# Performance work log

Hardware: AMD Instinct MI355X
Metric: run time of the kernel (lower is better)

Reference implementation:

```python
import jax, jax.numpy as jnp
import numpy as np

B, L, D = 32768, 256, 16  # batch, chain length, bond dim; physical dim d=2


def setup_inputs() -> dict:
    key = jax.random.key(0)
    k_phi, k_first, k_mid, k_last = jax.random.split(key, 4)
    scale = 1.0 / np.sqrt(2.0 * D)  # variance-preserving chain
    phi_batch = jax.random.normal(k_phi, (B, L, 2), dtype=jnp.float32)
    core_first = jax.random.normal(k_first, (2, D), dtype=jnp.float32) * scale
    cores_mid = jax.random.normal(k_mid, (L - 2, D, 2, D), dtype=jnp.float32) * scale
    core_last = jax.random.normal(k_last, (D, 2), dtype=jnp.float32) * scale
    out_bias = jnp.zeros((), dtype=jnp.float32)
    return {
        "phi_batch": phi_batch,
        "core_first": core_first,
        "cores_mid": cores_mid,
        "core_last": core_last,
        "out_bias": out_bias,
    }


def reference(phi_batch, core_first, cores_mid, core_last, out_bias):
    # MPS / tensor-train contraction, batched over samples.
    # Each sample contracts feature vectors phi[i] (len-2) into the physical
    # index of core i, then chains the resulting D x D matrices via a
    # left-to-right bond-space matvec (what cotengra would find per-sample).
    # v0: [B, D] = phi[:,0] contracted with first core [2, D]
    v0 = jnp.einsum("bp,pd->bd", phi_batch[:, 0], core_first)

    # middle features, scan-major layout: [L-2, B, 2]
    phis_mid = jnp.swapaxes(phi_batch[:, 1:-1], 0, 1)

    def step(v, xs):
        phi_t, core = xs  # phi_t: [B, 2], core: [D, 2, D]
        # contract bond then physical index; never materialize [B, D, D]
        u = jnp.einsum("bq,qpr->bpr", v, core)   # [B, 2, D]
        v_new = jnp.einsum("bp,bpr->br", phi_t, u)  # [B, D]
        return v_new, None

    v, _ = jax.lax.scan(step, v0, (phis_mid, cores_mid))

    # close the chain with last core [D, 2] and last feature [B, 2]
    out = jnp.einsum("bq,qp,bp->b", v, core_last, phi_batch[:, -1])
    return out + out_bias
```

## Files before the change

### kernel.cpp

```cpp
#include <hip/hip_runtime.h>
#include <stdint.h>


typedef short  bf16x8 __attribute__((ext_vector_type(8)));
typedef float  f32x4  __attribute__((ext_vector_type(4)));
typedef int    i32x4  __attribute__((ext_vector_type(4)));
typedef unsigned int u32;

#define NFWD 128
#define NBWD 126
#define BWD_OFF (NFWD*2*64)

#if __has_builtin(__builtin_amdgcn_perm)
#define PACK_HI(hi, lo) ((int)__builtin_amdgcn_perm((u32)(hi), (u32)(lo), 0x07060302u))
#else
#define PACK_HI(hi, lo) ((int)(((u32)(hi) & 0xFFFF0000u) | ((u32)(lo) >> 16)))
#endif

__device__ __forceinline__ u32 rne_bump(u32 u){
  return u + 0x7FFFu + ((u >> 16) & 1u);
}

__global__ void build_frags(const float* __restrict__ cm, i32x4* __restrict__ ws)
{
  const int bid  = blockIdx.x;
  const int p    = threadIdx.x >> 6;
  const int lane = threadIdx.x & 63;
  const int m    = lane & 15;
  const int g    = lane >> 4;
  const bool fwd = bid < NFWD;
  const int slot = fwd ? bid : (bid - NFWD);
  const int t    = fwd ? bid : (253 - slot);
  i32x4* dst = ws + (fwd ? 0 : BWD_OFF) + (slot*2 + p)*64 + lane;
  i32x4 w;
  #pragma unroll
  for(int d=0; d<4; ++d){
    u32 h[2];
    #pragma unroll
    for(int e=0; e<2; ++e){
      const int j = 2*d + e;
      const int k = g*8 + j;
      const int q = k & 15;
      const int lohalf = k >> 4;
      const int ci = fwd ? ((((t*16 + q)*2) + p)*16 + m)
                         : ((((t*16 + m)*2) + p)*16 + q);
      const float c = cm[ci];
      const u32 u  = __float_as_uint(c);
      const u32 a  = rne_bump(u);
      const float hif = __uint_as_float(a & 0xFFFF0000u);
      const u32 b  = rne_bump(__float_as_uint(c - hif));
      h[e] = lohalf ? (b >> 16) : (a >> 16);
    }
    w[d] = (int)(h[0] | (h[1] << 16));
  }
  *dst = w;
}

__global__ __launch_bounds__(256) void mps_chain(
  const float* __restrict__ phi,
  const float* __restrict__ core_first,
  const float* __restrict__ core_last,
  const float* __restrict__ bias,
  const i32x4* __restrict__ ws,
  float* __restrict__ out)
{
  const int lane = threadIdx.x & 63;
  const int wv   = threadIdx.x >> 6;
  const int b0   = blockIdx.x * 32;
  const int n    = lane & 15;
  const int g    = lane >> 4;
  const int s_in = (wv & 1)*16 + n;
  const bool isFwd = (wv < 2);
  const bool hiSel = (g < 2);
  const int addrA  = (n + 32*(g & 1)) << 2;
  const int addrB  = addrA + 64;

  const float* phiRow = phi + (size_t)(b0 + s_in) * 512;

  __shared__ float red[2][32][20];

  float v[4];
  i32x4 bfrag, bswap;

  auto make_bfrag = [&](){
    const u32 u0 = __float_as_uint(v[0]), u1 = __float_as_uint(v[1]);
    const u32 u2 = __float_as_uint(v[2]), u3 = __float_as_uint(v[3]);
    const float l0 = v[0] - __uint_as_float(u0 & 0xFFFF0000u);
    const float l1 = v[1] - __uint_as_float(u1 & 0xFFFF0000u);
    const float l2 = v[2] - __uint_as_float(u2 & 0xFFFF0000u);
    const float l3 = v[3] - __uint_as_float(u3 & 0xFFFF0000u);
    const int hp01 = PACK_HI(u1, u0);
    const int hp23 = PACK_HI(u3, u2);
    const int lp01 = PACK_HI(__float_as_uint(l1), __float_as_uint(l0));
    const int lp23 = PACK_HI(__float_as_uint(l3), __float_as_uint(l2));
    const int ah0 = __builtin_amdgcn_ds_bpermute(addrA, hp01);
    const int ah1 = __builtin_amdgcn_ds_bpermute(addrA, hp23);
    const int al0 = __builtin_amdgcn_ds_bpermute(addrA, lp01);
    const int al1 = __builtin_amdgcn_ds_bpermute(addrA, lp23);
    const int bh0 = __builtin_amdgcn_ds_bpermute(addrB, hp01);
    const int bh1 = __builtin_amdgcn_ds_bpermute(addrB, hp23);
    const int bl0 = __builtin_amdgcn_ds_bpermute(addrB, lp01);
    const int bl1 = __builtin_amdgcn_ds_bpermute(addrB, lp23);
    bfrag[0] = hiSel ? ah0 : al0;   bswap[0] = hiSel ? al0 : ah0;
    bfrag[1] = hiSel ? ah1 : al1;   bswap[1] = hiSel ? al1 : ah1;
    bfrag[2] = hiSel ? bh0 : bl0;   bswap[2] = hiSel ? bl0 : bh0;
    bfrag[3] = hiSel ? bh1 : bl1;   bswap[3] = hiSel ? bl1 : bh1;
  };

  auto step = [&](const i32x4& a0, const i32x4& a1, float phx, float phy){
    f32x4 acc0 = {0.f,0.f,0.f,0.f};
    f32x4 acc1 = {0.f,0.f,0.f,0.f};
    const bf16x8 bh = __builtin_bit_cast(bf16x8, bfrag);
    const bf16x8 bs = __builtin_bit_cast(bf16x8, bswap);
    acc0 = __builtin_amdgcn_mfma_f32_16x16x32_bf16(__builtin_bit_cast(bf16x8, a0), bh, acc0, 0,0,0);
    acc0 = __builtin_amdgcn_mfma_f32_16x16x32_bf16(__builtin_bit_cast(bf16x8, a0), bs, acc0, 0,0,0);
    acc1 = __builtin_amdgcn_mfma_f32_16x16x32_bf16(__builtin_bit_cast(bf16x8, a1), bh, acc1, 0,0,0);
    acc1 = __builtin_amdgcn_mfma_f32_16x16x32_bf16(__builtin_bit_cast(bf16x8, a1), bs, acc1, 0,0,0);
    v[0] = phx*acc0[0] + phy*acc1[0];
    v[1] = phx*acc0[1] + phy*acc1[1];
    v[2] = phx*acc0[2] + phy*acc1[2];
    v[3] = phx*acc0[3] + phy*acc1[3];
    make_bfrag();
  };

  if (isFwd){
    const i32x4* tab = ws;
    float4 f4a = *(const float4*)phiRow;
    #pragma unroll
    for(int reg=0; reg<4; ++reg){
      const int r = g*4 + reg;
      v[reg] = f4a.x * core_first[r] + f4a.y * core_first[16 + r];
    }
    make_bfrag();
    i32x4 P0 = tab[lane],       P1 = tab[64 + lane];
    i32x4 Q0 = tab[128 + lane], Q1 = tab[192 + lane];
    #pragma unroll 1
    for(int t = 0; t < NFWD; t += 2){
      const float4 f4n = *(const float4*)(phiRow + 2*(t+2));
      step(P0, P1, f4a.z, f4a.w);
      {
        const int sp = (t+2 < NFWD) ? (t+2) : (NFWD-1);
        P0 = tab[sp*128 + lane]; P1 = tab[sp*128 + 64 + lane];
      }
      step(Q0, Q1, f4n.x, f4n.y);
      {
        const int sq = (t+3 < NFWD) ? (t+3) : (NFWD-1);
        Q0 = tab[sq*128 + lane]; Q1 = tab[sq*128 + 64 + lane];
      }
      f4a = f4n;
    }
  } else {
    const i32x4* tab = ws + BWD_OFF;
    float4 f4a = *(const float4*)(phiRow + 508);
    #pragma unroll
    for(int reg=0; reg<4; ++reg){
      const int r = g*4 + reg;
      v[reg] = f4a.z * core_last[2*r] + f4a.w * core_last[2*r + 1];
    }
    make_bfrag();
    i32x4 P0 = tab[lane],       P1 = tab[64 + lane];
    i32x4 Q0 = tab[128 + lane], Q1 = tab[192 + lane];
    float cx = f4a.x, cy = f4a.y;
    #pragma unroll 1
    for(int s = 0; s < NBWD; s += 2){
      const float4 f4n = *(const float4*)(phiRow + 2*(252-s));
      step(P0, P1, cx, cy);
      {
        const int sp = (s+2 < NBWD) ? (s+2) : (NBWD-1);
        P0 = tab[sp*128 + lane]; P1 = tab[sp*128 + 64 + lane];
      }
      step(Q0, Q1, f4n.z, f4n.w);
      {
        const int sq = (s+3 < NBWD) ? (s+3) : (NBWD-1);
        Q0 = tab[sq*128 + lane]; Q1 = tab[sq*128 + 64 + lane];
      }
      cx = f4n.x; cy = f4n.y;
    }
  }

  *(float4*)&red[isFwd ? 0 : 1][s_in][4*g] = make_float4(v[0], v[1], v[2], v[3]);
  __syncthreads();
  if (threadIdx.x < 32){
    const int s = threadIdx.x;
    float acc = bias[0];
    #pragma unroll
    for(int q = 0; q < 16; ++q)
      acc += red[0][s][q] * red[1][s][q];
    out[b0 + s] = acc;
  }
}

extern "C" void kernel_launch(void* const* d_in, const int* in_sizes, int n_in,
                              void* d_out, int out_size, void* d_ws, size_t ws_size,
                              hipStream_t stream)
{
  const float* phi  = (const float*)d_in[0];
  const float* cf   = (const float*)d_in[1];
  const float* cm   = (const float*)d_in[2];
  const float* cl   = (const float*)d_in[3];
  const float* bias = (const float*)d_in[4];
  i32x4* ws = (i32x4*)d_ws;

  build_frags<<<254, 128, 0, stream>>>(cm, ws);
  mps_chain<<<1024, 256, 0, stream>>>(phi, cf, cl, bias, ws, (float*)d_out);
}
```

Measured before the change: 157.1 us.

## Reorder core fragment layout to drop cross-lane bpermutes in chain step

Changes the k-ordering of the prebuilt bf16 hi/lo core fragments so each lane's own packed vector values can feed the MFMA B operand directly. This removes the eight ds_bpermute shuffles and selects on the serial per-step critical path, which now only packs and swaps registers. The prefetch of core fragments and phi values is also deepened from two steps to four, with an explicit tail for the backward chain. The cost is more live registers and a new correctness dependency on the fragment layout matching the MFMA operand mapping.

```diff
diff --git a/kernel.cpp b/kernel.cpp
--- a/kernel.cpp
+++ b/kernel.cpp
@@ -11,11 +11,7 @@
 #define NBWD 126
 #define BWD_OFF (NFWD*2*64)
 
-#if __has_builtin(__builtin_amdgcn_perm)
 #define PACK_HI(hi, lo) ((int)__builtin_amdgcn_perm((u32)(hi), (u32)(lo), 0x07060302u))
-#else
-#define PACK_HI(hi, lo) ((int)(((u32)(hi) & 0xFFFF0000u) | ((u32)(lo) >> 16)))
-#endif
 
 __device__ __forceinline__ u32 rne_bump(u32 u){
   return u + 0x7FFFu + ((u >> 16) & 1u);
@@ -39,9 +35,8 @@
     #pragma unroll
     for(int e=0; e<2; ++e){
       const int j = 2*d + e;
-      const int k = g*8 + j;
-      const int q = k & 15;
-      const int lohalf = k >> 4;
+      const int q = 4*g + (j & 3);
+      const bool hi_part = (j < 4);
       const int ci = fwd ? ((((t*16 + q)*2) + p)*16 + m)
                          : ((((t*16 + m)*2) + p)*16 + q);
       const float c = cm[ci];
@@ -49,7 +44,7 @@
       const u32 a  = rne_bump(u);
       const float hif = __uint_as_float(a & 0xFFFF0000u);
       const u32 b  = rne_bump(__float_as_uint(c - hif));
-      h[e] = lohalf ? (b >> 16) : (a >> 16);
+      h[e] = hi_part ? (a >> 16) : (b >> 16);
     }
     w[d] = (int)(h[0] | (h[1] << 16));
   }
@@ -71,16 +66,13 @@
   const int g    = lane >> 4;
   const int s_in = (wv & 1)*16 + n;
   const bool isFwd = (wv < 2);
-  const bool hiSel = (g < 2);
-  const int addrA  = (n + 32*(g & 1)) << 2;
-  const int addrB  = addrA + 64;
 
   const float* phiRow = phi + (size_t)(b0 + s_in) * 512;
 
   __shared__ float red[2][32][20];
 
   float v[4];
-  i32x4 bfrag, bswap;
+  i32x4 bfr;
 
   auto make_bfrag = [&](){
     const u32 u0 = __float_as_uint(v[0]), u1 = __float_as_uint(v[1]);
@@ -89,29 +81,18 @@
     const float l1 = v[1] - __uint_as_float(u1 & 0xFFFF0000u);
     const float l2 = v[2] - __uint_as_float(u2 & 0xFFFF0000u);
     const float l3 = v[3] - __uint_as_float(u3 & 0xFFFF0000u);
-    const int hp01 = PACK_HI(u1, u0);
-    const int hp23 = PACK_HI(u3, u2);
-    const int lp01 = PACK_HI(__float_as_uint(l1), __float_as_uint(l0));
-    const int lp23 = PACK_HI(__float_as_uint(l3), __float_as_uint(l2));
-    const int ah0 = __builtin_amdgcn_ds_bpermute(addrA, hp01);
-    const int ah1 = __builtin_amdgcn_ds_bpermute(addrA, hp23);
-    const int al0 = __builtin_amdgcn_ds_bpermute(addrA, lp01);
-    const int al1 = __builtin_amdgcn_ds_bpermute(addrA, lp23);
-    const int bh0 = __builtin_amdgcn_ds_bpermute(addrB, hp01);
-    const int bh1 = __builtin_amdgcn_ds_bpermute(addrB, hp23);
-    const int bl0 = __builtin_amdgcn_ds_bpermute(addrB, lp01);
-    const int bl1 = __builtin_amdgcn_ds_bpermute(addrB, lp23);
-    bfrag[0] = hiSel ? ah0 : al0;   bswap[0] = hiSel ? al0 : ah0;
-    bfrag[1] = hiSel ? ah1 : al1;   bswap[1] = hiSel ? al1 : ah1;
-    bfrag[2] = hiSel ? bh0 : bl0;   bswap[2] = hiSel ? bl0 : bh0;
-    bfrag[3] = hiSel ? bh1 : bl1;   bswap[3] = hiSel ? bl1 : bh1;
+    bfr[0] = PACK_HI(u1, u0);
+    bfr[1] = PACK_HI(u3, u2);
+    bfr[2] = PACK_HI(__float_as_uint(l1), __float_as_uint(l0));
+    bfr[3] = PACK_HI(__float_as_uint(l3), __float_as_uint(l2));
   };
 
   auto step = [&](const i32x4& a0, const i32x4& a1, float phx, float phy){
+    i32x4 sw; sw[0]=bfr[2]; sw[1]=bfr[3]; sw[2]=bfr[0]; sw[3]=bfr[1];
+    const bf16x8 bh = __builtin_bit_cast(bf16x8, bfr);
+    const bf16x8 bs = __builtin_bit_cast(bf16x8, sw);
     f32x4 acc0 = {0.f,0.f,0.f,0.f};
     f32x4 acc1 = {0.f,0.f,0.f,0.f};
-    const bf16x8 bh = __builtin_bit_cast(bf16x8, bfrag);
-    const bf16x8 bs = __builtin_bit_cast(bf16x8, bswap);
     acc0 = __builtin_amdgcn_mfma_f32_16x16x32_bf16(__builtin_bit_cast(bf16x8, a0), bh, acc0, 0,0,0);
     acc0 = __builtin_amdgcn_mfma_f32_16x16x32_bf16(__builtin_bit_cast(bf16x8, a0), bs, acc0, 0,0,0);
     acc1 = __builtin_amdgcn_mfma_f32_16x16x32_bf16(__builtin_bit_cast(bf16x8, a1), bh, acc1, 0,0,0);
@@ -125,57 +106,78 @@
 
   if (isFwd){
     const i32x4* tab = ws;
-    float4 f4a = *(const float4*)phiRow;
+    const float2 ph0 = *(const float2*)phiRow;
     #pragma unroll
     for(int reg=0; reg<4; ++reg){
       const int r = g*4 + reg;
-      v[reg] = f4a.x * core_first[r] + f4a.y * core_first[16 + r];
+      v[reg] = ph0.x * core_first[r] + ph0.y * core_first[16 + r];
     }
     make_bfrag();
-    i32x4 P0 = tab[lane],       P1 = tab[64 + lane];
-    i32x4 Q0 = tab[128 + lane], Q1 = tab[192 + lane];
+    i32x4 F0a = tab[lane],       F0b = tab[64 + lane];
+    i32x4 F1a = tab[128 + lane], F1b = tab[192 + lane];
+    i32x4 F2a = tab[256 + lane], F2b = tab[320 + lane];
+    i32x4 F3a = tab[384 + lane], F3b = tab[448 + lane];
+    float2 c0 = *(const float2*)(phiRow + 2);
+    float2 c1 = *(const float2*)(phiRow + 4);
+    float2 c2 = *(const float2*)(phiRow + 6);
+    float2 c3 = *(const float2*)(phiRow + 8);
     #pragma unroll 1
-    for(int t = 0; t < NFWD; t += 2){
-      const float4 f4n = *(const float4*)(phiRow + 2*(t+2));
-      step(P0, P1, f4a.z, f4a.w);
-      {
-        const int sp = (t+2 < NFWD) ? (t+2) : (NFWD-1);
-        P0 = tab[sp*128 + lane]; P1 = tab[sp*128 + 64 + lane];
-      }
-      step(Q0, Q1, f4n.x, f4n.y);
-      {
-        const int sq = (t+3 < NFWD) ? (t+3) : (NFWD-1);
-        Q0 = tab[sq*128 + lane]; Q1 = tab[sq*128 + 64 + lane];
-      }
-      f4a = f4n;
+    for(int t = 0; t < NFWD; t += 4){
+      step(F0a, F0b, c0.x, c0.y);
+      { const int sp = (t+4 < NFWD) ? (t+4) : (NFWD-1);
+        F0a = tab[sp*128 + lane]; F0b = tab[sp*128 + 64 + lane];
+        c0 = *(const float2*)(phiRow + 2*(t+5)); }
+      step(F1a, F1b, c1.x, c1.y);
+      { const int sp = (t+5 < NFWD) ? (t+5) : (NFWD-1);
+        F1a = tab[sp*128 + lane]; F1b = tab[sp*128 + 64 + lane];
+        c1 = *(const float2*)(phiRow + 2*(t+6)); }
+      step(F2a, F2b, c2.x, c2.y);
+      { const int sp = (t+6 < NFWD) ? (t+6) : (NFWD-1);
+        F2a = tab[sp*128 + lane]; F2b = tab[sp*128 + 64 + lane];
+        c2 = *(const float2*)(phiRow + 2*(t+7)); }
+      step(F3a, F3b, c3.x, c3.y);
+      { const int sp = (t+7 < NFWD) ? (t+7) : (NFWD-1);
+        F3a = tab[sp*128 + lane]; F3b = tab[sp*128 + 64 + lane];
+        c3 = *(const float2*)(phiRow + 2*(t+8)); }
     }
   } else {
     const i32x4* tab = ws + BWD_OFF;
-    float4 f4a = *(const float4*)(phiRow + 508);
+    const float4 fL = *(const float4*)(phiRow + 508);
     #pragma unroll
     for(int reg=0; reg<4; ++reg){
       const int r = g*4 + reg;
-      v[reg] = f4a.z * core_last[2*r] + f4a.w * core_last[2*r + 1];
+      v[reg] = fL.z * core_last[2*r] + fL.w * core_last[2*r + 1];
     }
     make_bfrag();
-    i32x4 P0 = tab[lane],       P1 = tab[64 + lane];
-    i32x4 Q0 = tab[128 + lane], Q1 = tab[192 + lane];
-    float cx = f4a.x, cy = f4a.y;
+    i32x4 F0a = tab[lane],       F0b = tab[64 + lane];
+    i32x4 F1a = tab[128 + lane], F1b = tab[192 + lane];
+    i32x4 F2a = tab[256 + lane], F2b = tab[320 + lane];
+    i32x4 F3a = tab[384 + lane], F3b = tab[448 + lane];
+    float2 c0 = make_float2(fL.x, fL.y);
+    float2 c1 = *(const float2*)(phiRow + 2*253);
+    float2 c2 = *(const float2*)(phiRow + 2*252);
+    float2 c3 = *(const float2*)(phiRow + 2*251);
     #pragma unroll 1
-    for(int s = 0; s < NBWD; s += 2){
-      const float4 f4n = *(const float4*)(phiRow + 2*(252-s));
-      step(P0, P1, cx, cy);
-      {
-        const int sp = (s+2 < NBWD) ? (s+2) : (NBWD-1);
-        P0 = tab[sp*128 + lane]; P1 = tab[sp*128 + 64 + lane];
-      }
-      step(Q0, Q1, f4n.z, f4n.w);
-      {
-        const int sq = (s+3 < NBWD) ? (s+3) : (NBWD-1);
-        Q0 = tab[sq*128 + lane]; Q1 = tab[sq*128 + 64 + lane];
-      }
-      cx = f4n.x; cy = f4n.y;
-    }
+    for(int s = 0; s < 124; s += 4){
+      step(F0a, F0b, c0.x, c0.y);
+      { const int sp = (s+4 < NBWD) ? (s+4) : (NBWD-1);
+        F0a = tab[sp*128 + lane]; F0b = tab[sp*128 + 64 + lane];
+        c0 = *(const float2*)(phiRow + 2*(250-s)); }
+      step(F1a, F1b, c1.x, c1.y);
+      { const int sp = (s+5 < NBWD) ? (s+5) : (NBWD-1);
+        F1a = tab[sp*128 + lane]; F1b = tab[sp*128 + 64 + lane];
+        c1 = *(const float2*)(phiRow + 2*(249-s)); }
+      step(F2a, F2b, c2.x, c2.y);
+      { const int sp = (s+6 < NBWD) ? (s+6) : (NBWD-1);
+        F2a = tab[sp*128 + lane]; F2b = tab[sp*128 + 64 + lane];
+        c2 = *(const float2*)(phiRow + 2*(248-s)); }
+      step(F3a, F3b, c3.x, c3.y);
+      { const int sp = (s+7 < NBWD) ? (s+7) : (NBWD-1);
+        F3a = tab[sp*128 + lane]; F3b = tab[sp*128 + 64 + lane];
+        c3 = *(const float2*)(phiRow + 2*(247-s)); }
+    }
+    step(F0a, F0b, c0.x, c0.y);
+    step(F1a, F1b, c1.x, c1.y);
   }
 
   *(float4*)&red[isFwd ? 0 : 1][s_in][4*g] = make_float4(v[0], v[1], v[2], v[3]);
```

Result: slower. 160.6 us (+2.2%).
